# Optimization experiments

Hardware: AMD Instinct MI355X
Metric: run time of the kernel (lower is better)

## Reference

```python
import jax, jax.numpy as jnp
import numpy as np

# Config (mirrors HymbaLayer init + env constants)
DIM = 1024; NH = 16; NKV = 4; D = 64          # head_dim = DIM // NH
NATTN = NH // 2; NSSM = NH // 2; KVREP = NATTN // NKV
S = 16          # _HYMBA_SSM_STATE
NMETA = 4       # _HYMBA_META_TOK
BASE = 10000.0  # rope_base
CHUNK = 64      # _HYMBA_SCAN_CHUNK
B, T = 2, 2048


def _rms_norm(x, eps=1e-6):
    return x * jax.lax.rsqrt(jnp.mean(x * x, -1, keepdims=True) + eps)


def _rotary_cs(t_len, d, base):
    inv = 1.0 / (base ** (jnp.arange(0, d, 2, dtype=jnp.float32) / d))  # (d/2,)
    f = jnp.arange(t_len, dtype=jnp.float32)[:, None] * inv[None, :]    # (T, d/2)
    return jnp.cos(f), jnp.sin(f)


def _apply_rot(x, cos, sin):
    # x: (B, H, T, D); rotate-half style rotary
    d2 = x.shape[-1] // 2
    x1, x2 = x[..., :d2], x[..., d2:]
    c, s = cos[None, None], sin[None, None]
    return jnp.concatenate([x1 * c - x2 * s, x1 * s + x2 * c], -1)


def _scan_chunks(log_a, u, chunk):
    # Exact chunk-parallel diagonal scan: h_t = exp(log_a_t)*h_{t-1} + u_t
    b, t, s = u.shape
    nc = t // chunk
    la = log_a.reshape(b, nc, chunk, s)
    uu = u.reshape(b, nc, chunk, s)
    log_p = jnp.clip(jnp.cumsum(la, axis=2), -30.0, 0.0)
    p = jnp.exp(log_p)
    h_local = p * jnp.cumsum(uu * jnp.exp(-log_p), axis=2)

    def step(h0, args):
        hl, pc = args                          # (B, chunk, S)
        hc = hl + pc * h0[:, None, :]
        return hc[:, -1], hc

    _, hs = jax.lax.scan(step, jnp.zeros((b, s), u.dtype),
                         (jnp.swapaxes(h_local, 0, 1), jnp.swapaxes(p, 0, 1)))
    return jnp.swapaxes(hs, 0, 1).reshape(b, t, s)


def _mamba_head(logA, Bw, Cw, dtw, dtb, Ow, x):
    # x: (B, T, D); selective SSM with diagonal A
    dt = jnp.minimum(jax.nn.softplus(x @ dtw.T + dtb), 1.0)   # (B,T,S)
    A = jnp.minimum(-jnp.exp(logA), 10.0)                      # (S,)
    log_a = jnp.clip(dt * A, -0.5, 0.0)
    Bx = (x @ Bw.T) * dt
    Cc = x @ Cw.T
    h = _scan_chunks(log_a, Bx, CHUNK)                         # (B,T,S)
    y = jnp.sum(Cc * h, -1, keepdims=True)
    return h @ Ow.T + y * x[..., :1]


def _forward(x, meta_tokens, c_q_w, c_k_w, c_v_w, q_gain, ssm_in_w, proj_w,
             attn_scale, ssm_scale, ssm_logA, ssm_Bw, ssm_Cw, ssm_dtw, ssm_dtb, ssm_Ow):
    b, t, c = x.shape
    x_ext = jnp.concatenate([jnp.broadcast_to(meta_tokens, (b, NMETA, c)), x], 1)
    t_ext = t + NMETA
    q = (x_ext @ c_q_w.T).reshape(b, t_ext, NH, D).transpose(0, 2, 1, 3)
    k = (x_ext @ c_k_w.T).reshape(b, t_ext, NKV, D).transpose(0, 2, 1, 3)
    v = (x_ext @ c_v_w.T).reshape(b, t_ext, NKV, D).transpose(0, 2, 1, 3)
    q = _rms_norm(q); k = _rms_norm(k)
    cos, sin = _rotary_cs(t_ext, D, BASE)
    q = _apply_rot(q, cos, sin); k = _apply_rot(k, cos, sin)
    # GQA attention over the first NATTN heads, causal over T_ext
    q_attn = q[:, :NATTN] * q_gain[None, :, None, None]
    k_exp = jnp.repeat(k, KVREP, axis=1)
    v_exp = jnp.repeat(v, KVREP, axis=1)
    scores = jnp.einsum('bhqd,bhkd->bhqk', q_attn, k_exp) / jnp.sqrt(jnp.float32(D))
    mask = jnp.tril(jnp.ones((t_ext, t_ext), bool))
    scores = jnp.where(mask[None, None], scores, -jnp.inf)
    attn = jax.nn.softmax(scores, axis=-1)
    ao = jnp.einsum('bhqk,bhkd->bhqd', attn, v_exp)
    ao = ao[:, :, NMETA:].transpose(0, 2, 1, 3).reshape(b, t, NATTN * D) * attn_scale
    # SSM branch on the original (un-prepended) tokens
    ssm_x = (x @ ssm_in_w.T).reshape(b, t, NSSM, D)
    ssm_out = jax.vmap(_mamba_head, in_axes=(0, 0, 0, 0, 0, 0, 2), out_axes=2)(
        ssm_logA, ssm_Bw, ssm_Cw, ssm_dtw, ssm_dtb, ssm_Ow, ssm_x)
    ssm_out = ssm_out.reshape(b, t, NSSM * D) * ssm_scale
    return jnp.concatenate([ao, ssm_out], -1) @ proj_w.T


def setup_inputs() -> dict:
    key = jax.random.key(0)
    ks = jax.random.split(key, 16)
    r = lambda k, sh, sc=0.02: jax.random.normal(k, sh, jnp.float32) * sc
    return {
        'x': jax.random.normal(ks[0], (B, T, DIM), jnp.float32),
        'meta_tokens': r(ks[1], (1, NMETA, DIM)),
        'c_q_w': r(ks[2], (DIM, DIM)),
        'c_k_w': r(ks[3], (NKV * D, DIM)),
        'c_v_w': r(ks[4], (NKV * D, DIM)),
        'q_gain': jnp.full((NATTN,), 1.0, jnp.float32),
        'ssm_in_w': r(ks[5], (NSSM * D, DIM)),
        'proj_w': r(ks[6], (DIM, DIM)),
        'attn_scale': jnp.ones((1,), jnp.float32),
        'ssm_scale': jnp.ones((1,), jnp.float32),
        'ssm_logA': jax.random.normal(ks[7], (NSSM, S), jnp.float32) * 0.5,
        'ssm_Bw': r(ks[8], (NSSM, S, D), 0.05),
        'ssm_Cw': r(ks[9], (NSSM, S, D), 0.05),
        'ssm_dtw': r(ks[10], (NSSM, S, D), 0.05),
        'ssm_dtb': jnp.full((NSSM, S), -4.0, jnp.float32),
        'ssm_Ow': r(ks[11], (NSSM, D, S), 0.05),
    }


def reference(x, meta_tokens, c_q_w, c_k_w, c_v_w, q_gain, ssm_in_w, proj_w,
              attn_scale, ssm_scale, ssm_logA, ssm_Bw, ssm_Cw, ssm_dtw, ssm_dtb, ssm_Ow):
    return _forward(x, meta_tokens, c_q_w, c_k_w, c_v_w, q_gain, ssm_in_w, proj_w,
                    attn_scale, ssm_scale, ssm_logA, ssm_Bw, ssm_Cw, ssm_dtw, ssm_dtb, ssm_Ow)
```

## Files before the change

kernel.cpp:

```cpp
#include <hip/hip_runtime.h>
#include <hip/hip_bf16.h>
#include <math.h>

typedef __hip_bfloat16 bf16;
typedef __attribute__((ext_vector_type(8))) short short8;
typedef __attribute__((ext_vector_type(4))) float f32x4;

static constexpr int kB = 2;
static constexpr int kT = 2048;
static constexpr int kDIM = 1024;
static constexpr int kNMETA = 4;
static constexpr int kTEXT = kT + kNMETA;
static constexpr int kMEXT = kB * kTEXT;
static constexpr int kMPAD = 4224;
static constexpr int kMX = kB * kT;
static constexpr int kQT = 33;
static constexpr int kTP = 2112;

static constexpr size_t oXE = 0;
static constexpr size_t oYB = 0;
static constexpr size_t oQB = 8650752;
static constexpr size_t oKB = oQB + (size_t)kMPAD * 512 * 2;
static constexpr size_t oVB = oKB + (size_t)kMPAD * 256 * 2;
static constexpr size_t oLA = oQB;
static constexpr size_t oUU = oLA + (size_t)kMX * 128 * 4;
static constexpr size_t oCC = oUU + (size_t)kMX * 128 * 4;
static constexpr size_t oHL = oCC + (size_t)kMX * 128 * 4;
static constexpr size_t oPB = oHL + (size_t)kMX * 128 * 2;
static constexpr size_t oCH = oPB + (size_t)kMX * 128 * 2;
static constexpr size_t oCP = oCH + 16384 * 4;
static constexpr size_t oH0 = oCP + 16384 * 4;
static constexpr size_t oSX = oVB + (size_t)kMPAD * 256 * 2;
static constexpr size_t oQP = oSX + (size_t)kMX * 512 * 2;
static constexpr size_t oKP = oQP + (size_t)kB * 8 * kTP * 64 * 2;
static constexpr size_t oVT = oKP + (size_t)kB * 4 * kTP * 64 * 2;
static constexpr size_t oWQ = oQP;
static constexpr size_t oWP = oVT + (size_t)kB * 4 * 64 * kTP * 2;
static constexpr size_t oAO = 33554432;
static constexpr size_t oAL = oAO + (size_t)2 * kB * 8 * kTP * 64 * 4;

#define GLD_LDS16(gp, lp)                                                          \
  __builtin_amdgcn_global_load_lds((const __attribute__((address_space(1))) void*)(gp), \
                                   (__attribute__((address_space(3))) void*)(lp), 16, 0, 0)

__device__ __forceinline__ uint4 pack8(float4 a, float4 b) {
  union { bf16 h[8]; uint4 v; } u;
  u.h[0] = __float2bfloat16(a.x); u.h[1] = __float2bfloat16(a.y);
  u.h[2] = __float2bfloat16(a.z); u.h[3] = __float2bfloat16(a.w);
  u.h[4] = __float2bfloat16(b.x); u.h[5] = __float2bfloat16(b.y);
  u.h[6] = __float2bfloat16(b.z); u.h[7] = __float2bfloat16(b.w);
  return u.v;
}

__global__ __launch_bounds__(256) void prep_all(const float* __restrict__ cq, const float* __restrict__ ck,
                                                const float* __restrict__ cv, const float* __restrict__ sw,
                                                const float* __restrict__ pw,
                                                const float* __restrict__ x, const float* __restrict__ meta,
                                                bf16* __restrict__ wqkvsx, bf16* __restrict__ wproj,
                                                bf16* __restrict__ xe) {
  int i = blockIdx.x * 256 + threadIdx.x;
  int row = i >> 7, v = i & 127;
  if (row < 2560) {
    const float* src; bf16* dst;
    if (row < 512)       { src = cq + (size_t)row * 1024;          dst = wqkvsx + (size_t)row * 1024; }
    else if (row < 768)  { src = ck + (size_t)(row - 512) * 1024;  dst = wqkvsx + (size_t)row * 1024; }
    else if (row < 1024) { src = cv + (size_t)(row - 768) * 1024;  dst = wqkvsx + (size_t)row * 1024; }
    else if (row < 1536) { src = sw + (size_t)(row - 1024) * 1024; dst = wqkvsx + (size_t)row * 1024; }
    else                 { src = pw + (size_t)(row - 1536) * 1024; dst = wproj + (size_t)(row - 1536) * 1024; }
    float4 a0 = ((const float4*)src)[v * 2], a1 = ((const float4*)src)[v * 2 + 1];
    ((uint4*)dst)[v] = pack8(a0, a1);
  } else {
    int r = row - 2560;
    if (r >= kMPAD) return;
    uint4 val = {0u, 0u, 0u, 0u};
    if (r < kMEXT) {
      int b = r / kTEXT, te = r - b * kTEXT;
      const float* src = (te < kNMETA) ? (meta + (size_t)te * kDIM)
                                       : (x + ((size_t)b * kT + (te - kNMETA)) * kDIM);
      float4 a0 = ((const float4*)src)[v * 2];
      float4 a1 = ((const float4*)src)[v * 2 + 1];
      val = pack8(a0, a1);
    }
    ((uint4*)(xe + (size_t)r * kDIM))[v] = val;
  }
}

template <int MODE>
__global__ __launch_bounds__(256) void gemm_t(const bf16* __restrict__ A,
                                              const bf16* __restrict__ W,
                                              void* __restrict__ O0, void* __restrict__ O1,
                                              void* __restrict__ O2, void* __restrict__ O3) {
  __shared__ short As[128 * 32];
  __shared__ short Bs[64 * 32];
  const int tid = threadIdx.x;
  const int wave = tid >> 6, lane = tid & 63;
  const int quad = lane >> 4, l16 = lane & 15;
  const int bm = blockIdx.y * 128, bn = blockIdx.x * 64;
  const int srow = tid >> 2, scol = (tid & 3) * 8;
  const bf16* ag0 = A + (size_t)(bm + srow) * 1024 + scol;
  const bf16* ag1 = A + (size_t)(bm + 64 + srow) * 1024 + scol;
  const bf16* bg0 = W + (size_t)(bn + srow) * 1024 + scol;
  char* asb = (char*)As + wave * 1024;
  char* bsb = (char*)Bs + wave * 1024;
  f32x4 acc[2][4] = {};
  for (int k0 = 0; k0 < 1024; k0 += 32) {
    __syncthreads();
    GLD_LDS16(ag0, asb);
    GLD_LDS16(ag1, asb + 4096);
    GLD_LDS16(bg0, bsb);
    ag0 += 32; ag1 += 32; bg0 += 32;
    __syncthreads();
    short8 af[2], bfr[4];
#pragma unroll
    for (int mi = 0; mi < 2; ++mi)
      af[mi] = *(const short8*)((const char*)As + (size_t)(wave * 32 + mi * 16 + l16) * 64 + quad * 16);
#pragma unroll
    for (int ni = 0; ni < 4; ++ni)
      bfr[ni] = *(const short8*)((const char*)Bs + (size_t)(ni * 16 + l16) * 64 + quad * 16);
#pragma unroll
    for (int mi = 0; mi < 2; ++mi)
#pragma unroll
      for (int ni = 0; ni < 4; ++ni)
        acc[mi][ni] = __builtin_amdgcn_mfma_f32_16x16x32_bf16(af[mi], bfr[ni], acc[mi][ni], 0, 0, 0);
  }
#pragma unroll
  for (int mi = 0; mi < 2; ++mi)
#pragma unroll
    for (int ni = 0; ni < 4; ++ni) {
      int colg = bn + ni * 16 + l16;
#pragma unroll
      for (int r = 0; r < 4; ++r) {
        int row = bm + wave * 32 + mi * 16 + quad * 4 + r;
        float val = acc[mi][ni][r];
        if constexpr (MODE == 2) {
          ((float*)O0)[(size_t)row * 1024 + colg] = val;
        } else {
          if (colg < 512)       ((bf16*)O0)[(size_t)row * 512 + colg]        = __float2bfloat16(val);
          else if (colg < 768)  ((bf16*)O1)[(size_t)row * 256 + colg - 512]  = __float2bfloat16(val);
          else if (colg < 1024) ((bf16*)O2)[(size_t)row * 256 + colg - 768]  = __float2bfloat16(val);
          else if (row < kMEXT) {
            int bb = row >= kTEXT ? 1 : 0;
            int te = row - bb * kTEXT;
            if (te >= kNMETA)
              ((bf16*)O3)[((size_t)(bb * kT + te - kNMETA)) * 512 + colg - 1024] = __float2bfloat16(val);
          }
        }
      }
    }
}

__global__ __launch_bounds__(256) void norm_rope_pack(const bf16* __restrict__ QB,
                                                      const bf16* __restrict__ KB,
                                                      const float* __restrict__ q_gain,
                                                      bf16* __restrict__ Qp, bf16* __restrict__ Kp) {
  int job = blockIdx.x * 4 + (threadIdx.x >> 6);
  if (job >= kB * kTP * 12) return;
  int lane = threadIdx.x & 63;
  int slot = job % 12, rowp = job / 12;
  int b = rowp / kTP, te = rowp % kTP;
  bf16* dst = (slot < 8) ? Qp + (((size_t)(b * 8 + slot)) * kTP + te) * 64 + lane
                         : Kp + (((size_t)(b * 4 + slot - 8)) * kTP + te) * 64 + lane;
  if (te >= kTEXT) { *dst = __float2bfloat16(0.f); return; }
  const bf16* src = (slot < 8) ? QB + ((size_t)(b * kTEXT + te)) * 512 + slot * 64 + lane
                               : KB + ((size_t)(b * kTEXT + te)) * 256 + (slot - 8) * 64 + lane;
  float v = __bfloat162float(*src);
  float ss = v * v;
#pragma unroll
  for (int o = 32; o > 0; o >>= 1) ss += __shfl_xor(ss, o, 64);
  float vn = v * (1.f / sqrtf(ss * (1.f / 64.f) + 1e-6f));
  float p = __shfl_xor(vn, 32, 64);
  float ang = (float)te * exp2f(-13.287712379549449f * (float)(lane & 31) * (1.f / 32.f));
  float c = __cosf(ang), s = __sinf(ang);
  float outv = (lane < 32) ? (vn * c - p * s) : (p * s + vn * c);
  float gain = (slot < 8) ? q_gain[slot] * 0.125f : 1.f;
  *dst = __float2bfloat16(outv * gain);
}

__global__ __launch_bounds__(256) void vrepack(const bf16* __restrict__ VB, bf16* __restrict__ Vt) {
  __shared__ short Ts[64][66];
  const int tt = blockIdx.x, kvh = blockIdx.y, b = blockIdx.z;
  const int tid = threadIdx.x;
#pragma unroll
  for (int r = 0; r < 2; ++r) {
    int e = r * 256 + tid, row = e >> 3, c8 = e & 7;
    int te = tt * 64 + row;
    uint4 val = {0u, 0u, 0u, 0u};
    if (te < kTEXT) val = *(const uint4*)(VB + ((size_t)(b * kTEXT + te)) * 256 + kvh * 64 + c8 * 8);
    union { uint4 u; short s[8]; } w; w.u = val;
#pragma unroll
    for (int i = 0; i < 8; ++i) Ts[row][c8 * 8 + i] = w.s[i];
  }
  __syncthreads();
#pragma unroll
  for (int r = 0; r < 2; ++r) {
    int e = r * 256 + tid, d = e >> 3, c8 = e & 7;
    union { uint4 u; short s[8]; } w;
#pragma unroll
    for (int i = 0; i < 8; ++i) w.s[i] = Ts[c8 * 8 + i][d];
    *(uint4*)(Vt + (((size_t)(b * 4 + kvh)) * 64 + d) * kTP + tt * 64 + c8 * 8) = w.u;
  }
}

__global__ __launch_bounds__(256) void attn_part(const bf16* __restrict__ Qp,
                                                 const bf16* __restrict__ Kp,
                                                 const bf16* __restrict__ Vt,
                                                 float* __restrict__ AO, float* __restrict__ AL) {
  __shared__ short Ks[64][72];
  __shared__ short Vs[64][72];
  __shared__ short Ps[4][16][72];
  const int part = blockIdx.x & 1;
  const int qt = (kQT - 1) - (blockIdx.x >> 1);
  const int h = blockIdx.y, b = blockIdx.z;
  const int kvh = h >> 1;
  const int tid = threadIdx.x, wave = tid >> 6, lane = tid & 63;
  const int quad = lane >> 4, l16 = lane & 15;
  const int hsplit = (qt + 2) >> 1;
  const int kt_begin = part == 0 ? 0 : hsplit;
  const int kt_end = part == 0 ? hsplit : qt + 1;

  short8 qf[2];
  {
    const bf16* qrow = Qp + (((size_t)(b * 8 + h)) * kTP + qt * 64 + wave * 16 + l16) * 64 + quad * 8;
    qf[0] = *(const short8*)(qrow);
    qf[1] = *(const short8*)(qrow + 32);
  }
  short8 ones;
#pragma unroll
  for (int i = 0; i < 8; ++i) ones[i] = (short)0x3F80;

  const bf16* kbase = Kp + ((size_t)(b * 4 + kvh)) * kTP * 64;
  const bf16* vbase = Vt + ((size_t)(b * 4 + kvh)) * 64 * kTP;

  const int r0row = tid >> 3, r0c8 = tid & 7;
  const int r1row = (256 + tid) >> 3, r1c8 = tid & 7;

  f32x4 O[4] = {};
  f32x4 lacc = {};
  const int q_abs = qt * 64 + wave * 16 + l16;

  uint4 kr0 = *(const uint4*)(kbase + (size_t)(kt_begin * 64 + r0row) * 64 + r0c8 * 8);
  uint4 kr1 = *(const uint4*)(kbase + (size_t)(kt_begin * 64 + r1row) * 64 + r1c8 * 8);
  uint4 vr0 = *(const uint4*)(vbase + (size_t)r0row * kTP + kt_begin * 64 + r0c8 * 8);
  uint4 vr1 = *(const uint4*)(vbase + (size_t)r1row * kTP + kt_begin * 64 + r1c8 * 8);

  for (int kt = kt_begin; kt < kt_end; ++kt) {
    __syncthreads();
    *(uint4*)&Ks[r0row][r0c8 * 8] = kr0;
    *(uint4*)&Ks[r1row][r1c8 * 8] = kr1;
    *(uint4*)&Vs[r0row][r0c8 * 8] = vr0;
    *(uint4*)&Vs[r1row][r1c8 * 8] = vr1;
    if (kt + 1 < kt_end) {
      int kn = (kt + 1) * 64;
      kr0 = *(const uint4*)(kbase + (size_t)(kn + r0row) * 64 + r0c8 * 8);
      kr1 = *(const uint4*)(kbase + (size_t)(kn + r1row) * 64 + r1c8 * 8);
      vr0 = *(const uint4*)(vbase + (size_t)r0row * kTP + kn + r0c8 * 8);
      vr1 = *(const uint4*)(vbase + (size_t)r1row * kTP + kn + r1c8 * 8);
    }
    __syncthreads();

    f32x4 st[4] = {};
#pragma unroll
    for (int nb = 0; nb < 4; ++nb) {
      short8 ak0 = *(const short8*)&Ks[nb * 16 + l16][quad * 8];
      st[nb] = __builtin_amdgcn_mfma_f32_16x16x32_bf16(ak0, qf[0], st[nb], 0, 0, 0);
      short8 ak1 = *(const short8*)&Ks[nb * 16 + l16][32 + quad * 8];
      st[nb] = __builtin_amdgcn_mfma_f32_16x16x32_bf16(ak1, qf[1], st[nb], 0, 0, 0);
    }
    if (kt == qt) {
      int key0 = kt * 64 + quad * 4;
#pragma unroll
      for (int nb = 0; nb < 4; ++nb)
#pragma unroll
        for (int rg = 0; rg < 4; ++rg)
          if (key0 + nb * 16 + rg > q_abs) st[nb][rg] = -1e30f;
    }
#pragma unroll
    for (int nb = 0; nb < 4; ++nb) {
      union { unsigned long long q; bf16 hh[4]; } pw;
#pragma unroll
      for (int rg = 0; rg < 4; ++rg) pw.hh[rg] = __float2bfloat16(__expf(st[nb][rg]));
      *(unsigned long long*)&Ps[wave][l16][nb * 16 + quad * 4] = pw.q;
    }
    short8 pf0 = *(const short8*)&Ps[wave][l16][quad * 8];
    short8 pf1 = *(const short8*)&Ps[wave][l16][32 + quad * 8];
    lacc = __builtin_amdgcn_mfma_f32_16x16x32_bf16(pf0, ones, lacc, 0, 0, 0);
    lacc = __builtin_amdgcn_mfma_f32_16x16x32_bf16(pf1, ones, lacc, 0, 0, 0);
#pragma unroll
    for (int db = 0; db < 4; ++db) {
      short8 bv0 = *(const short8*)&Vs[db * 16 + l16][quad * 8];
      O[db] = __builtin_amdgcn_mfma_f32_16x16x32_bf16(pf0, bv0, O[db], 0, 0, 0);
      short8 bv1 = *(const short8*)&Vs[db * 16 + l16][32 + quad * 8];
      O[db] = __builtin_amdgcn_mfma_f32_16x16x32_bf16(pf1, bv1, O[db], 0, 0, 0);
    }
  }
  size_t hb = (((size_t)part * 2 + b) * 8 + h);
  float* aoB = AO + hb * kTP * 64;
  float* alB = AL + hb * kTP;
#pragma unroll
  for (int rg = 0; rg < 4; ++rg) {
    int q = qt * 64 + wave * 16 + quad * 4 + rg;
    float* dst = aoB + (size_t)q * 64 + l16;
#pragma unroll
    for (int db = 0; db < 4; ++db) dst[db * 16] = O[db][rg];
    if (l16 == 0) alB[q] = lacc[rg];
  }
}

__global__ __launch_bounds__(256) void attn_combine(const float* __restrict__ AO,
                                                    const float* __restrict__ AL,
                                                    const float* __restrict__ attn_scale,
                                                    bf16* __restrict__ Y) {
  int id = blockIdx.x * 256 + threadIdx.x;
  int d16 = id & 3;
  int tmp = id >> 2;
  int q = tmp % kTP; tmp /= kTP;
  int h = tmp & 7, b = tmp >> 3;
  if (q < kNMETA || q >= kTEXT) return;
  size_t hb0 = ((size_t)b * 8 + h), hb1 = ((size_t)(2 + b) * 8 + h);
  float l = AL[hb0 * kTP + q] + AL[hb1 * kTP + q];
  float so = attn_scale[0] / fmaxf(l, 1e-30f);
  const float4* p0 = (const float4*)(AO + (hb0 * kTP + q) * 64 + d16 * 16);
  const float4* p1 = (const float4*)(AO + (hb1 * kTP + q) * 64 + d16 * 16);
  bf16* dst = Y + ((size_t)(b * kT + q - kNMETA)) * kDIM + h * 64 + d16 * 16;
#pragma unroll
  for (int i = 0; i < 4; ++i) {
    float4 a = p0[i], c = p1[i];
    dst[i * 4 + 0] = __float2bfloat16((a.x + c.x) * so);
    dst[i * 4 + 1] = __float2bfloat16((a.y + c.y) * so);
    dst[i * 4 + 2] = __float2bfloat16((a.z + c.z) * so);
    dst[i * 4 + 3] = __float2bfloat16((a.w + c.w) * so);
  }
}

__global__ __launch_bounds__(256) void ssm_prep(const bf16* __restrict__ sx,
                                                const float* __restrict__ dtw, const float* __restrict__ dtb,
                                                const float* __restrict__ Bw, const float* __restrict__ Cw,
                                                const float* __restrict__ logA,
                                                float* __restrict__ la, float* __restrict__ u,
                                                float* __restrict__ Cc) {
  __shared__ short Xs[64][72];
  __shared__ short Ws[48][72];
  const int bm = blockIdx.x * 64, h = blockIdx.y;
  const int tid = threadIdx.x, wave = tid >> 6, lane = tid & 63;
  const int quad = lane >> 4, l16 = lane & 15;
#pragma unroll
  for (int is = 0; is < 2; ++is) {
    int e = is * 256 + tid;
    int row = e >> 3, v = e & 7;
    uint4 val = *(const uint4*)(sx + ((size_t)(bm + row)) * 512 + h * 64 + v * 8);
    *(uint4*)&Xs[row][v * 8] = val;
  }
#pragma unroll
  for (int is = 0; is < 2; ++is) {
    int s = is * 256 + tid;
    if (s < 384) {
      int row = s >> 3, v = s & 7;
      const float* src = (row < 16) ? dtw + ((size_t)(h * 16 + row)) * 64
                       : (row < 32) ? Bw + ((size_t)(h * 16 + row - 16)) * 64
                                    : Cw + ((size_t)(h * 16 + row - 32)) * 64;
      float4 a0 = ((const float4*)src)[v * 2];
      float4 a1 = ((const float4*)src)[v * 2 + 1];
      *(uint4*)&Ws[row][v * 8] = pack8(a0, a1);
    }
  }
  __syncthreads();
  short8 af0 = *(const short8*)&Xs[wave * 16 + l16][quad * 8];
  short8 af1 = *(const short8*)&Xs[wave * 16 + l16][32 + quad * 8];
  f32x4 acc[3] = {};
#pragma unroll
  for (int nb = 0; nb < 3; ++nb) {
    short8 b0 = *(const short8*)&Ws[nb * 16 + l16][quad * 8];
    acc[nb] = __builtin_amdgcn_mfma_f32_16x16x32_bf16(af0, b0, acc[nb], 0, 0, 0);
    short8 b1 = *(const short8*)&Ws[nb * 16 + l16][32 + quad * 8];
    acc[nb] = __builtin_amdgcn_mfma_f32_16x16x32_bf16(af1, b1, acc[nb], 0, 0, 0);
  }
  float dtb_v = dtb[h * 16 + l16];
  float A_v = fminf(-expf(logA[h * 16 + l16]), 10.f);
#pragma unroll
  for (int rg = 0; rg < 4; ++rg) {
    int bt = bm + wave * 16 + quad * 4 + rg;
    size_t ix = (size_t)bt * 128 + h * 16 + l16;
    float raw = acc[0][rg] + dtb_v;
    float sp = fmaxf(raw, 0.f) + log1pf(expf(-fabsf(raw)));
    float dt = fminf(sp, 1.f);
    float lav = fminf(fmaxf(dt * A_v, -0.5f), 0.f);
    la[ix] = lav;
    u[ix] = acc[1][rg] * dt;
    Cc[ix] = acc[2][rg];
  }
}

__global__ __launch_bounds__(256) void ssm_scan1(const float* __restrict__ la, const float* __restrict__ u,
                                                 bf16* __restrict__ hloc, bf16* __restrict__ Pb,
                                                 float* __restrict__ chHt, float* __restrict__ chPt) {
  int id = blockIdx.x * 256 + threadIdx.x;
  if (id >= 16384) return;
  int hs = id & 127, c = (id >> 7) & 63, b = id >> 13;
  float hv = 0.f, cum = 0.f;
  size_t base = ((size_t)b * kT) * 128 + hs;
  for (int i = 0; i < 32; ++i) {
    size_t ix = base + (size_t)(c * 32 + i) * 128;
    float lav = la[ix], uv = u[ix];
    cum += lav;
    hv = expf(lav) * hv + uv;
    hloc[ix] = __float2bfloat16(hv);
    Pb[ix] = __float2bfloat16(expf(fmaxf(cum, -30.f)));
  }
  int t = b * 8192 + hs * 64 + c;
  chHt[t] = hv;
  chPt[t] = expf(fmaxf(cum, -30.f));
}

__global__ __launch_bounds__(256) void ssm_scan2(const float* __restrict__ chHt,
                                                 const float* __restrict__ chPt,
                                                 float* __restrict__ h0) {
  int id = blockIdx.x * 256 + threadIdx.x;
  int c = id & 63;
  int chain = id >> 6;
  int b = chain >> 7, hs = chain & 127;
  int t = b * 8192 + hs * 64 + c;
  float H = chHt[t], P = chPt[t];
#pragma unroll
  for (int off = 1; off < 64; off <<= 1) {
    float Hp = __shfl_up(H, off, 64);
    float Pp = __shfl_up(P, off, 64);
    if (c >= off) { H = H + P * Hp; P = P * Pp; }
  }
  float Hex = __shfl_up(H, 1, 64);
  if (c == 0) Hex = 0.f;
  h0[b * 8192 + c * 128 + hs] = Hex;
}

__global__ __launch_bounds__(256) void ssm_out(const bf16* __restrict__ hloc, const bf16* __restrict__ Pb,
                                               const float* __restrict__ h0, const float* __restrict__ Cc,
                                               const bf16* __restrict__ sx, const float* __restrict__ Ow,
                                               const float* __restrict__ ssm_scale, bf16* __restrict__ Y) {
  int id = blockIdx.x * 256 + threadIdx.x;
  if (id >= kMX * 32) return;
  int d4 = id & 3, h = (id >> 2) & 7, t = (id >> 5) & 2047, b = id >> 16;
  size_t ix0 = ((size_t)(b * kT + t)) * 128 + h * 16;
  int h0b = b * 8192 + (t >> 5) * 128 + h * 16;
  float hv[16], y = 0.f;
#pragma unroll
  for (int s = 0; s < 16; ++s) {
    float v = __bfloat162float(hloc[ix0 + s]) + __bfloat162float(Pb[ix0 + s]) * h0[h0b + s];
    hv[s] = v;
    y += Cc[ix0 + s] * v;
  }
  float x0 = __bfloat162float(sx[((size_t)(b * kT + t)) * 512 + h * 64]);
  float scl = ssm_scale[0];
  const float* ow = Ow + ((size_t)h * 64 + d4 * 16) * 16;
  bf16* dst = Y + ((size_t)(b * kT + t)) * kDIM + 512 + h * 64 + d4 * 16;
  float yx = y * x0;
#pragma unroll
  for (int d = 0; d < 16; ++d) {
    float acc = yx;
    const float* owr = ow + d * 16;
#pragma unroll
    for (int s = 0; s < 16; ++s) acc += hv[s] * owr[s];
    dst[d] = __float2bfloat16(acc * scl);
  }
}

extern "C" void kernel_launch(void* const* d_in, const int* in_sizes, int n_in,
                              void* d_out, int out_size, void* d_ws, size_t ws_size,
                              hipStream_t stream) {
  (void)in_sizes; (void)n_in; (void)out_size; (void)ws_size;
  const float* x        = (const float*)d_in[0];
  const float* meta     = (const float*)d_in[1];
  const float* c_q_w    = (const float*)d_in[2];
  const float* c_k_w    = (const float*)d_in[3];
  const float* c_v_w    = (const float*)d_in[4];
  const float* q_gain   = (const float*)d_in[5];
  const float* ssm_in_w = (const float*)d_in[6];
  const float* proj_w   = (const float*)d_in[7];
  const float* attn_sc  = (const float*)d_in[8];
  const float* ssm_sc   = (const float*)d_in[9];
  const float* ssm_logA = (const float*)d_in[10];
  const float* ssm_Bw   = (const float*)d_in[11];
  const float* ssm_Cw   = (const float*)d_in[12];
  const float* ssm_dtw  = (const float*)d_in[13];
  const float* ssm_dtb  = (const float*)d_in[14];
  const float* ssm_Ow   = (const float*)d_in[15];

  char* w = (char*)d_ws;
  bf16*  XE = (bf16*)(w + oXE);
  bf16*  QB = (bf16*)(w + oQB);
  bf16*  KB = (bf16*)(w + oKB);
  bf16*  VB = (bf16*)(w + oVB);
  bf16*  SX = (bf16*)(w + oSX);
  bf16*  YB = (bf16*)(w + oYB);
  bf16*  QP = (bf16*)(w + oQP);
  bf16*  KP = (bf16*)(w + oKP);
  bf16*  VT = (bf16*)(w + oVT);
  bf16*  WQ = (bf16*)(w + oWQ);
  bf16*  WP = (bf16*)(w + oWP);
  float* LA = (float*)(w + oLA);
  float* UU = (float*)(w + oUU);
  float* CC = (float*)(w + oCC);
  bf16*  HL = (bf16*)(w + oHL);
  bf16*  PB = (bf16*)(w + oPB);
  float* CH = (float*)(w + oCH);
  float* CP = (float*)(w + oCP);
  float* H0 = (float*)(w + oH0);
  float* AO = (float*)(w + oAO);
  float* AL = (float*)(w + oAL);

  prep_all<<<(2560 + kMPAD) * 128 / 256, 256, 0, stream>>>(c_q_w, c_k_w, c_v_w, ssm_in_w, proj_w,
                                                           x, meta, WQ, WP, XE);

  gemm_t<0><<<dim3(24, kMPAD / 128), 256, 0, stream>>>(XE, WQ, QB, KB, VB, SX);

  norm_rope_pack<<<(kB * kTP * 12) / 4, 256, 0, stream>>>(QB, KB, q_gain, QP, KP);
  vrepack<<<dim3(kQT, 4, kB), 256, 0, stream>>>(VB, VT);

  attn_part<<<dim3(kQT * 2, 8, kB), 256, 0, stream>>>(QP, KP, VT, AO, AL);
  attn_combine<<<(2 * 8 * kTP * 4) / 256, 256, 0, stream>>>(AO, AL, attn_sc, YB);

  ssm_prep<<<dim3(kMX / 64, 8), 256, 0, stream>>>(SX, ssm_dtw, ssm_dtb, ssm_Bw, ssm_Cw,
                                                  ssm_logA, LA, UU, CC);
  ssm_scan1<<<64, 256, 0, stream>>>(LA, UU, HL, PB, CH, CP);
  ssm_scan2<<<64, 256, 0, stream>>>(CH, CP, H0);
  ssm_out<<<kMX * 32 / 256, 256, 0, stream>>>(HL, PB, H0, CC, SX, ssm_Ow, ssm_sc, YB);

  gemm_t<2><<<dim3(16, kMX / 128), 256, 0, stream>>>(YB, WP, d_out, nullptr, nullptr, nullptr);
}
```

Measured before the change: 231.5 us.

## Fuse RMS-norm, rotary and V transpose into QKV GEMM epilogue; merge combine kernels

The QKV GEMM epilogue now applies RMS norm, q_gain scaling and rotary directly on the accumulators. It writes Q and K straight into the padded per-head layout and stores V transposed, which removes the norm_rope_pack and vrepack kernels and their intermediate buffers. Padding rows are zeroed in prep_all, attention-combine and SSM output are merged into one launch, and la/u are interleaved as float2. This cuts kernel launches and global round trips at the cost of scattered narrow stores in the GEMM epilogue and a reworked workspace layout.

```diff
diff --git a/kernel.cpp b/kernel.cpp
--- a/kernel.cpp
+++ b/kernel.cpp
@@ -19,24 +19,20 @@
 
 static constexpr size_t oXE = 0;
 static constexpr size_t oYB = 0;
-static constexpr size_t oQB = 8650752;
-static constexpr size_t oKB = oQB + (size_t)kMPAD * 512 * 2;
-static constexpr size_t oVB = oKB + (size_t)kMPAD * 256 * 2;
-static constexpr size_t oLA = oQB;
-static constexpr size_t oUU = oLA + (size_t)kMX * 128 * 4;
-static constexpr size_t oCC = oUU + (size_t)kMX * 128 * 4;
+static constexpr size_t oLU = 8650752;
+static constexpr size_t oCC = oLU + (size_t)kMX * 128 * 8;
 static constexpr size_t oHL = oCC + (size_t)kMX * 128 * 4;
 static constexpr size_t oPB = oHL + (size_t)kMX * 128 * 2;
 static constexpr size_t oCH = oPB + (size_t)kMX * 128 * 2;
 static constexpr size_t oCP = oCH + 16384 * 4;
 static constexpr size_t oH0 = oCP + 16384 * 4;
-static constexpr size_t oSX = oVB + (size_t)kMPAD * 256 * 2;
+static constexpr size_t oSX = oLU + (size_t)kMX * 128 * 8 + (size_t)kMX * 128 * 12;
 static constexpr size_t oQP = oSX + (size_t)kMX * 512 * 2;
 static constexpr size_t oKP = oQP + (size_t)kB * 8 * kTP * 64 * 2;
 static constexpr size_t oVT = oKP + (size_t)kB * 4 * kTP * 64 * 2;
-static constexpr size_t oWQ = oQP;
 static constexpr size_t oWP = oVT + (size_t)kB * 4 * 64 * kTP * 2;
-static constexpr size_t oAO = 33554432;
+static constexpr size_t oWQ = oWP + (size_t)1024 * 1024 * 2;
+static constexpr size_t oAO = 100663296;
 static constexpr size_t oAL = oAO + (size_t)2 * kB * 8 * kTP * 64 * 4;
 
 #define GLD_LDS16(gp, lp)                                                          \
@@ -57,10 +53,12 @@
                                                 const float* __restrict__ pw,
                                                 const float* __restrict__ x, const float* __restrict__ meta,
                                                 bf16* __restrict__ wqkvsx, bf16* __restrict__ wproj,
-                                                bf16* __restrict__ xe) {
+                                                bf16* __restrict__ xe,
+                                                bf16* __restrict__ Qp, bf16* __restrict__ Kp,
+                                                bf16* __restrict__ Vt) {
   int i = blockIdx.x * 256 + threadIdx.x;
-  int row = i >> 7, v = i & 127;
-  if (row < 2560) {
+  if (i < 327680) {
+    int row = i >> 7, v = i & 127;
     const float* src; bf16* dst;
     if (row < 512)       { src = cq + (size_t)row * 1024;          dst = wqkvsx + (size_t)row * 1024; }
     else if (row < 768)  { src = ck + (size_t)(row - 512) * 1024;  dst = wqkvsx + (size_t)row * 1024; }
@@ -69,9 +67,9 @@
     else                 { src = pw + (size_t)(row - 1536) * 1024; dst = wproj + (size_t)(row - 1536) * 1024; }
     float4 a0 = ((const float4*)src)[v * 2], a1 = ((const float4*)src)[v * 2 + 1];
     ((uint4*)dst)[v] = pack8(a0, a1);
-  } else {
-    int r = row - 2560;
-    if (r >= kMPAD) return;
+  } else if (i < 868352) {
+    int j = i - 327680;
+    int r = j >> 7, v = j & 127;
     uint4 val = {0u, 0u, 0u, 0u};
     if (r < kMEXT) {
       int b = r / kTEXT, te = r - b * kTEXT;
@@ -82,6 +80,20 @@
       val = pack8(a0, a1);
     }
     ((uint4*)(xe + (size_t)r * kDIM))[v] = val;
+  } else {
+    int j = i - 868352;
+    if (j < 30720) {
+      int k = j & 31, te = (j >> 5) % 60, bh = j / (60 * 32);
+      *(unsigned int*)(Qp + ((size_t)bh * kTP + 2052 + te) * 64 + k * 2) = 0u;
+    } else if (j < 46080) {
+      int jj = j - 30720;
+      int k = jj & 31, te = (jj >> 5) % 60, bh = jj / (60 * 32);
+      *(unsigned int*)(Kp + ((size_t)bh * kTP + 2052 + te) * 64 + k * 2) = 0u;
+    } else if (j < 61440) {
+      int jj = j - 46080;
+      int k = jj % 30, rowd = jj / 30;
+      *(unsigned int*)(Vt + (size_t)rowd * kTP + 2052 + k * 2) = 0u;
+    }
   }
 }
 
@@ -89,7 +101,8 @@
 __global__ __launch_bounds__(256) void gemm_t(const bf16* __restrict__ A,
                                               const bf16* __restrict__ W,
                                               void* __restrict__ O0, void* __restrict__ O1,
-                                              void* __restrict__ O2, void* __restrict__ O3) {
+                                              void* __restrict__ O2, void* __restrict__ O3,
+                                              const float* __restrict__ q_gain) {
   __shared__ short As[128 * 32];
   __shared__ short Bs[64 * 32];
   const int tid = threadIdx.x;
@@ -123,81 +136,90 @@
       for (int ni = 0; ni < 4; ++ni)
         acc[mi][ni] = __builtin_amdgcn_mfma_f32_16x16x32_bf16(af[mi], bfr[ni], acc[mi][ni], 0, 0, 0);
   }
-#pragma unroll
-  for (int mi = 0; mi < 2; ++mi)
-#pragma unroll
-    for (int ni = 0; ni < 4; ++ni) {
-      int colg = bn + ni * 16 + l16;
-#pragma unroll
-      for (int r = 0; r < 4; ++r) {
-        int row = bm + wave * 32 + mi * 16 + quad * 4 + r;
-        float val = acc[mi][ni][r];
-        if constexpr (MODE == 2) {
-          ((float*)O0)[(size_t)row * 1024 + colg] = val;
+  if constexpr (MODE == 2) {
+#pragma unroll
+    for (int mi = 0; mi < 2; ++mi)
+#pragma unroll
+      for (int ni = 0; ni < 4; ++ni) {
+        int colg = bn + ni * 16 + l16;
+#pragma unroll
+        for (int r = 0; r < 4; ++r) {
+          int row = bm + wave * 32 + mi * 16 + quad * 4 + r;
+          ((float*)O0)[(size_t)row * 1024 + colg] = acc[mi][ni][r];
+        }
+      }
+  } else {
+    const int tile = blockIdx.x;
+    if (tile < 16) {
+      float gain = (tile < 8) ? q_gain[tile] * 0.125f : 1.f;
+      float inv0 = exp2f(-13.287712379549449f * (float)l16 * (1.f / 32.f));
+      float inv1 = exp2f(-13.287712379549449f * (float)(l16 + 16) * (1.f / 32.f));
+#pragma unroll
+      for (int mi = 0; mi < 2; ++mi) {
+        int row0 = bm + wave * 32 + mi * 16 + quad * 4;
+        if (row0 >= kMEXT) continue;
+        int b = row0 >= kTEXT ? 1 : 0;
+        int te0 = row0 - b * kTEXT;
+        if (tile < 12) {
+          float ss[4];
+#pragma unroll
+          for (int r = 0; r < 4; ++r) {
+            float s = 0.f;
+#pragma unroll
+            for (int ni = 0; ni < 4; ++ni) s += acc[mi][ni][r] * acc[mi][ni][r];
+#pragma unroll
+            for (int off = 1; off < 16; off <<= 1) s += __shfl_xor(s, off, 64);
+            ss[r] = s;
+          }
+          bf16* base = (tile < 8)
+            ? (bf16*)O0 + (((size_t)(b * 8 + tile)) * kTP + te0) * 64 + l16
+            : (bf16*)O1 + (((size_t)(b * 4 + tile - 8)) * kTP + te0) * 64 + l16;
+#pragma unroll
+          for (int r = 0; r < 4; ++r) {
+            float rn = rsqrtf(ss[r] * (1.f / 64.f) + 1e-6f) * gain;
+            float te = (float)(te0 + r);
+            float a0 = te * inv0, a1 = te * inv1;
+            float c0 = __cosf(a0), s0 = __sinf(a0);
+            float c1 = __cosf(a1), s1 = __sinf(a1);
+            float v0 = acc[mi][0][r] * rn, v1 = acc[mi][1][r] * rn;
+            float v2 = acc[mi][2][r] * rn, v3 = acc[mi][3][r] * rn;
+            bf16* dst = base + (size_t)r * 64;
+            dst[0]  = __float2bfloat16(v0 * c0 - v2 * s0);
+            dst[16] = __float2bfloat16(v1 * c1 - v3 * s1);
+            dst[32] = __float2bfloat16(v0 * s0 + v2 * c0);
+            dst[48] = __float2bfloat16(v1 * s1 + v3 * c1);
+          }
         } else {
-          if (colg < 512)       ((bf16*)O0)[(size_t)row * 512 + colg]        = __float2bfloat16(val);
-          else if (colg < 768)  ((bf16*)O1)[(size_t)row * 256 + colg - 512]  = __float2bfloat16(val);
-          else if (colg < 1024) ((bf16*)O2)[(size_t)row * 256 + colg - 768]  = __float2bfloat16(val);
-          else if (row < kMEXT) {
-            int bb = row >= kTEXT ? 1 : 0;
-            int te = row - bb * kTEXT;
-            if (te >= kNMETA)
-              ((bf16*)O3)[((size_t)(bb * kT + te - kNMETA)) * 512 + colg - 1024] = __float2bfloat16(val);
+          int hv = tile - 12;
+#pragma unroll
+          for (int ni = 0; ni < 4; ++ni) {
+            union { unsigned long long q; bf16 hh[4]; } pw;
+#pragma unroll
+            for (int r = 0; r < 4; ++r) pw.hh[r] = __float2bfloat16(acc[mi][ni][r]);
+            *(unsigned long long*)((bf16*)O2 +
+                (((size_t)(b * 4 + hv)) * 64 + ni * 16 + l16) * kTP + te0) = pw.q;
           }
         }
       }
-    }
-}
-
-__global__ __launch_bounds__(256) void norm_rope_pack(const bf16* __restrict__ QB,
-                                                      const bf16* __restrict__ KB,
-                                                      const float* __restrict__ q_gain,
-                                                      bf16* __restrict__ Qp, bf16* __restrict__ Kp) {
-  int job = blockIdx.x * 4 + (threadIdx.x >> 6);
-  if (job >= kB * kTP * 12) return;
-  int lane = threadIdx.x & 63;
-  int slot = job % 12, rowp = job / 12;
-  int b = rowp / kTP, te = rowp % kTP;
-  bf16* dst = (slot < 8) ? Qp + (((size_t)(b * 8 + slot)) * kTP + te) * 64 + lane
-                         : Kp + (((size_t)(b * 4 + slot - 8)) * kTP + te) * 64 + lane;
-  if (te >= kTEXT) { *dst = __float2bfloat16(0.f); return; }
-  const bf16* src = (slot < 8) ? QB + ((size_t)(b * kTEXT + te)) * 512 + slot * 64 + lane
-                               : KB + ((size_t)(b * kTEXT + te)) * 256 + (slot - 8) * 64 + lane;
-  float v = __bfloat162float(*src);
-  float ss = v * v;
-#pragma unroll
-  for (int o = 32; o > 0; o >>= 1) ss += __shfl_xor(ss, o, 64);
-  float vn = v * (1.f / sqrtf(ss * (1.f / 64.f) + 1e-6f));
-  float p = __shfl_xor(vn, 32, 64);
-  float ang = (float)te * exp2f(-13.287712379549449f * (float)(lane & 31) * (1.f / 32.f));
-  float c = __cosf(ang), s = __sinf(ang);
-  float outv = (lane < 32) ? (vn * c - p * s) : (p * s + vn * c);
-  float gain = (slot < 8) ? q_gain[slot] * 0.125f : 1.f;
-  *dst = __float2bfloat16(outv * gain);
-}
-
-__global__ __launch_bounds__(256) void vrepack(const bf16* __restrict__ VB, bf16* __restrict__ Vt) {
-  __shared__ short Ts[64][66];
-  const int tt = blockIdx.x, kvh = blockIdx.y, b = blockIdx.z;
-  const int tid = threadIdx.x;
-#pragma unroll
-  for (int r = 0; r < 2; ++r) {
-    int e = r * 256 + tid, row = e >> 3, c8 = e & 7;
-    int te = tt * 64 + row;
-    uint4 val = {0u, 0u, 0u, 0u};
-    if (te < kTEXT) val = *(const uint4*)(VB + ((size_t)(b * kTEXT + te)) * 256 + kvh * 64 + c8 * 8);
-    union { uint4 u; short s[8]; } w; w.u = val;
-#pragma unroll
-    for (int i = 0; i < 8; ++i) Ts[row][c8 * 8 + i] = w.s[i];
-  }
-  __syncthreads();
-#pragma unroll
-  for (int r = 0; r < 2; ++r) {
-    int e = r * 256 + tid, d = e >> 3, c8 = e & 7;
-    union { uint4 u; short s[8]; } w;
-#pragma unroll
-    for (int i = 0; i < 8; ++i) w.s[i] = Ts[c8 * 8 + i][d];
-    *(uint4*)(Vt + (((size_t)(b * 4 + kvh)) * 64 + d) * kTP + tt * 64 + c8 * 8) = w.u;
+    } else {
+#pragma unroll
+      for (int mi = 0; mi < 2; ++mi)
+#pragma unroll
+        for (int ni = 0; ni < 4; ++ni) {
+          int colg = bn - 1024 + ni * 16 + l16;
+#pragma unroll
+          for (int r = 0; r < 4; ++r) {
+            int row = bm + wave * 32 + mi * 16 + quad * 4 + r;
+            if (row < kMEXT) {
+              int bb = row >= kTEXT ? 1 : 0;
+              int te = row - bb * kTEXT;
+              if (te >= kNMETA)
+                ((bf16*)O3)[((size_t)(bb * kT + te - kNMETA)) * 512 + colg] =
+                    __float2bfloat16(acc[mi][ni][r]);
+            }
+          }
+        }
+    }
   }
 }
 
@@ -306,38 +328,11 @@
   }
 }
 
-__global__ __launch_bounds__(256) void attn_combine(const float* __restrict__ AO,
-                                                    const float* __restrict__ AL,
-                                                    const float* __restrict__ attn_scale,
-                                                    bf16* __restrict__ Y) {
-  int id = blockIdx.x * 256 + threadIdx.x;
-  int d16 = id & 3;
-  int tmp = id >> 2;
-  int q = tmp % kTP; tmp /= kTP;
-  int h = tmp & 7, b = tmp >> 3;
-  if (q < kNMETA || q >= kTEXT) return;
-  size_t hb0 = ((size_t)b * 8 + h), hb1 = ((size_t)(2 + b) * 8 + h);
-  float l = AL[hb0 * kTP + q] + AL[hb1 * kTP + q];
-  float so = attn_scale[0] / fmaxf(l, 1e-30f);
-  const float4* p0 = (const float4*)(AO + (hb0 * kTP + q) * 64 + d16 * 16);
-  const float4* p1 = (const float4*)(AO + (hb1 * kTP + q) * 64 + d16 * 16);
-  bf16* dst = Y + ((size_t)(b * kT + q - kNMETA)) * kDIM + h * 64 + d16 * 16;
-#pragma unroll
-  for (int i = 0; i < 4; ++i) {
-    float4 a = p0[i], c = p1[i];
-    dst[i * 4 + 0] = __float2bfloat16((a.x + c.x) * so);
-    dst[i * 4 + 1] = __float2bfloat16((a.y + c.y) * so);
-    dst[i * 4 + 2] = __float2bfloat16((a.z + c.z) * so);
-    dst[i * 4 + 3] = __float2bfloat16((a.w + c.w) * so);
-  }
-}
-
 __global__ __launch_bounds__(256) void ssm_prep(const bf16* __restrict__ sx,
                                                 const float* __restrict__ dtw, const float* __restrict__ dtb,
                                                 const float* __restrict__ Bw, const float* __restrict__ Cw,
                                                 const float* __restrict__ logA,
-                                                float* __restrict__ la, float* __restrict__ u,
-                                                float* __restrict__ Cc) {
+                                                float* __restrict__ LU, float* __restrict__ Cc) {
   __shared__ short Xs[64][72];
   __shared__ short Ws[48][72];
   const int bm = blockIdx.x * 64, h = blockIdx.y;
@@ -384,13 +379,12 @@
     float sp = fmaxf(raw, 0.f) + log1pf(expf(-fabsf(raw)));
     float dt = fminf(sp, 1.f);
     float lav = fminf(fmaxf(dt * A_v, -0.5f), 0.f);
-    la[ix] = lav;
-    u[ix] = acc[1][rg] * dt;
+    *(float2*)(LU + 2 * ix) = make_float2(lav, acc[1][rg] * dt);
     Cc[ix] = acc[2][rg];
   }
 }
 
-__global__ __launch_bounds__(256) void ssm_scan1(const float* __restrict__ la, const float* __restrict__ u,
+__global__ __launch_bounds__(256) void ssm_scan1(const float* __restrict__ LU,
                                                  bf16* __restrict__ hloc, bf16* __restrict__ Pb,
                                                  float* __restrict__ chHt, float* __restrict__ chPt) {
   int id = blockIdx.x * 256 + threadIdx.x;
@@ -398,11 +392,12 @@
   int hs = id & 127, c = (id >> 7) & 63, b = id >> 13;
   float hv = 0.f, cum = 0.f;
   size_t base = ((size_t)b * kT) * 128 + hs;
+  const float2* LU2 = (const float2*)LU;
   for (int i = 0; i < 32; ++i) {
     size_t ix = base + (size_t)(c * 32 + i) * 128;
-    float lav = la[ix], uv = u[ix];
-    cum += lav;
-    hv = expf(lav) * hv + uv;
+    float2 lu = LU2[ix];
+    cum += lu.x;
+    hv = expf(lu.x) * hv + lu.y;
     hloc[ix] = __float2bfloat16(hv);
     Pb[ix] = __float2bfloat16(expf(fmaxf(cum, -30.f)));
   }
@@ -431,34 +426,60 @@
   h0[b * 8192 + c * 128 + hs] = Hex;
 }
 
-__global__ __launch_bounds__(256) void ssm_out(const bf16* __restrict__ hloc, const bf16* __restrict__ Pb,
-                                               const float* __restrict__ h0, const float* __restrict__ Cc,
-                                               const bf16* __restrict__ sx, const float* __restrict__ Ow,
-                                               const float* __restrict__ ssm_scale, bf16* __restrict__ Y) {
-  int id = blockIdx.x * 256 + threadIdx.x;
-  if (id >= kMX * 32) return;
-  int d4 = id & 3, h = (id >> 2) & 7, t = (id >> 5) & 2047, b = id >> 16;
-  size_t ix0 = ((size_t)(b * kT + t)) * 128 + h * 16;
-  int h0b = b * 8192 + (t >> 5) * 128 + h * 16;
-  float hv[16], y = 0.f;
-#pragma unroll
-  for (int s = 0; s < 16; ++s) {
-    float v = __bfloat162float(hloc[ix0 + s]) + __bfloat162float(Pb[ix0 + s]) * h0[h0b + s];
-    hv[s] = v;
-    y += Cc[ix0 + s] * v;
-  }
-  float x0 = __bfloat162float(sx[((size_t)(b * kT + t)) * 512 + h * 64]);
-  float scl = ssm_scale[0];
-  const float* ow = Ow + ((size_t)h * 64 + d4 * 16) * 16;
-  bf16* dst = Y + ((size_t)(b * kT + t)) * kDIM + 512 + h * 64 + d4 * 16;
-  float yx = y * x0;
-#pragma unroll
-  for (int d = 0; d < 16; ++d) {
-    float acc = yx;
-    const float* owr = ow + d * 16;
-#pragma unroll
-    for (int s = 0; s < 16; ++s) acc += hv[s] * owr[s];
-    dst[d] = __float2bfloat16(acc * scl);
+__global__ __launch_bounds__(256) void combine_out(const float* __restrict__ AO,
+                                                   const float* __restrict__ AL,
+                                                   const float* __restrict__ attn_scale,
+                                                   const bf16* __restrict__ hloc, const bf16* __restrict__ Pb,
+                                                   const float* __restrict__ h0, const float* __restrict__ Cc,
+                                                   const bf16* __restrict__ sx, const float* __restrict__ Ow,
+                                                   const float* __restrict__ ssm_scale,
+                                                   bf16* __restrict__ Y) {
+  if (blockIdx.x < 528) {
+    int id = blockIdx.x * 256 + threadIdx.x;
+    int d16 = id & 3;
+    int tmp = id >> 2;
+    int q = tmp % kTP; tmp /= kTP;
+    int h = tmp & 7, b = tmp >> 3;
+    if (q < kNMETA || q >= kTEXT) return;
+    size_t hb0 = ((size_t)b * 8 + h), hb1 = ((size_t)(2 + b) * 8 + h);
+    float l = AL[hb0 * kTP + q] + AL[hb1 * kTP + q];
+    float so = attn_scale[0] / fmaxf(l, 1e-30f);
+    const float4* p0 = (const float4*)(AO + (hb0 * kTP + q) * 64 + d16 * 16);
+    const float4* p1 = (const float4*)(AO + (hb1 * kTP + q) * 64 + d16 * 16);
+    bf16* dst = Y + ((size_t)(b * kT + q - kNMETA)) * kDIM + h * 64 + d16 * 16;
+#pragma unroll
+    for (int i = 0; i < 4; ++i) {
+      float4 a = p0[i], c = p1[i];
+      dst[i * 4 + 0] = __float2bfloat16((a.x + c.x) * so);
+      dst[i * 4 + 1] = __float2bfloat16((a.y + c.y) * so);
+      dst[i * 4 + 2] = __float2bfloat16((a.z + c.z) * so);
+      dst[i * 4 + 3] = __float2bfloat16((a.w + c.w) * so);
+    }
+  } else {
+    int id = (blockIdx.x - 528) * 256 + threadIdx.x;
+    int d4 = id & 3, h = (id >> 2) & 7, t = (id >> 5) & 2047, b = id >> 16;
+    size_t ix0 = ((size_t)(b * kT + t)) * 128 + h * 16;
+    int h0b = b * 8192 + (t >> 5) * 128 + h * 16;
+    float hv[16], y = 0.f;
+#pragma unroll
+    for (int s = 0; s < 16; ++s) {
+      float v = __bfloat162float(hloc[ix0 + s]) + __bfloat162float(Pb[ix0 + s]) * h0[h0b + s];
+      hv[s] = v;
+      y += Cc[ix0 + s] * v;
+    }
+    float x0 = __bfloat162float(sx[((size_t)(b * kT + t)) * 512 + h * 64]);
+    float scl = ssm_scale[0];
+    const float* ow = Ow + ((size_t)h * 64 + d4 * 16) * 16;
+    bf16* dst = Y + ((size_t)(b * kT + t)) * kDIM + 512 + h * 64 + d4 * 16;
+    float yx = y * x0;
+#pragma unroll
+    for (int d = 0; d < 16; ++d) {
+      float acc = yx;
+      const float* owr = ow + d * 16;
+#pragma unroll
+      for (int s = 0; s < 16; ++s) acc += hv[s] * owr[s];
+      dst[d] = __float2bfloat16(acc * scl);
+    }
   }
 }
 
@@ -485,9 +506,6 @@
 
   char* w = (char*)d_ws;
   bf16*  XE = (bf16*)(w + oXE);
-  bf16*  QB = (bf16*)(w + oQB);
-  bf16*  KB = (bf16*)(w + oKB);
-  bf16*  VB = (bf16*)(w + oVB);
   bf16*  SX = (bf16*)(w + oSX);
   bf16*  YB = (bf16*)(w + oYB);
   bf16*  QP = (bf16*)(w + oQP);
@@ -495,8 +513,7 @@
   bf16*  VT = (bf16*)(w + oVT);
   bf16*  WQ = (bf16*)(w + oWQ);
   bf16*  WP = (bf16*)(w + oWP);
-  float* LA = (float*)(w + oLA);
-  float* UU = (float*)(w + oUU);
+  float* LU = (float*)(w + oLU);
   float* CC = (float*)(w + oCC);
   bf16*  HL = (bf16*)(w + oHL);
   bf16*  PB = (bf16*)(w + oPB);
@@ -506,22 +523,19 @@
   float* AO = (float*)(w + oAO);
   float* AL = (float*)(w + oAL);
 
-  prep_all<<<(2560 + kMPAD) * 128 / 256, 256, 0, stream>>>(c_q_w, c_k_w, c_v_w, ssm_in_w, proj_w,
-                                                           x, meta, WQ, WP, XE);
-
-  gemm_t<0><<<dim3(24, kMPAD / 128), 256, 0, stream>>>(XE, WQ, QB, KB, VB, SX);
-
-  norm_rope_pack<<<(kB * kTP * 12) / 4, 256, 0, stream>>>(QB, KB, q_gain, QP, KP);
-  vrepack<<<dim3(kQT, 4, kB), 256, 0, stream>>>(VB, VT);
+  prep_all<<<3632, 256, 0, stream>>>(c_q_w, c_k_w, c_v_w, ssm_in_w, proj_w,
+                                     x, meta, WQ, WP, XE, QP, KP, VT);
+
+  gemm_t<0><<<dim3(24, kMPAD / 128), 256, 0, stream>>>(XE, WQ, QP, KP, VT, SX, q_gain);
 
   attn_part<<<dim3(kQT * 2, 8, kB), 256, 0, stream>>>(QP, KP, VT, AO, AL);
-  attn_combine<<<(2 * 8 * kTP * 4) / 256, 256, 0, stream>>>(AO, AL, attn_sc, YB);
 
   ssm_prep<<<dim3(kMX / 64, 8), 256, 0, stream>>>(SX, ssm_dtw, ssm_dtb, ssm_Bw, ssm_Cw,
-                                                  ssm_logA, LA, UU, CC);
-  ssm_scan1<<<64, 256, 0, stream>>>(LA, UU, HL, PB, CH, CP);
+                                                  ssm_logA, LU, CC);
+  ssm_scan1<<<64, 256, 0, stream>>>(LU, HL, PB, CH, CP);
   ssm_scan2<<<64, 256, 0, stream>>>(CH, CP, H0);
-  ssm_out<<<kMX * 32 / 256, 256, 0, stream>>>(HL, PB, H0, CC, SX, ssm_Ow, ssm_sc, YB);
-
-  gemm_t<2><<<dim3(16, kMX / 128), 256, 0, stream>>>(YB, WP, d_out, nullptr, nullptr, nullptr);
-}
+
+  combine_out<<<1040, 256, 0, stream>>>(AO, AL, attn_sc, HL, PB, H0, CC, SX, ssm_Ow, ssm_sc, YB);
+
+  gemm_t<2><<<dim3(16, kMX / 128), 256, 0, stream>>>(YB, WP, d_out, nullptr, nullptr, nullptr, nullptr);
+}
```

Result: faster. 215.7 us (-6.8%).
